# Performance work log

Hardware: AMD Instinct MI355X
Metric: run time of the kernel (lower is better)

The kernel has to match this reference:

```python
import jax, jax.numpy as jnp
import numpy as np

IN_FEATURES = 2048
HIDDEN_DIM = 1024
ENC_DIM = 1024
DEC_DIM = IN_FEATURES - ENC_DIM
MASK_VAL = -50000.0


def setup_inputs() -> dict:
    key = jax.random.key(0)
    k1, k2, k3, k4, k5 = jax.random.split(key, 5)
    B, S = 32, 2048
    encoder_outputs = jax.random.normal(k1, (B, S, ENC_DIM), dtype=jnp.float32)
    decoder_state = jax.random.normal(k2, (B, DEC_DIM), dtype=jnp.float32)
    # lengths in [1, S]
    sequence_length = jax.random.randint(k3, (B,), 1, S + 1).astype(jnp.int64)
    # fc_w: Linear(in_features, hidden_dim, bias=False) -> weight [hidden, in_feat]
    W = jax.random.normal(k4, (HIDDEN_DIM, IN_FEATURES), dtype=jnp.float32) / np.sqrt(IN_FEATURES)
    # fc_v: Linear(hidden_dim, 1, bias=False) -> weight [1, hidden]; store as [hidden]
    v = jax.random.normal(k5, (HIDDEN_DIM,), dtype=jnp.float32) / np.sqrt(HIDDEN_DIM)
    return {"encoder_outputs": encoder_outputs, "sequence_length": sequence_length,
            "decoder_state": decoder_state, "W": W, "v": v}


def reference(encoder_outputs, sequence_length, decoder_state, W, v):
    # score = v^T tanh(W [h; s]) == v^T tanh(W_enc h + W_dec s)  (avoids concat)
    W_enc = W[:, :ENC_DIM]      # [H, De]
    W_dec = W[:, ENC_DIM:]      # [H, Dd]
    # [B, S, H] + [B, 1, H]
    hidden = jnp.tanh(jnp.einsum('bse,he->bsh', encoder_outputs, W_enc)
                      + jnp.einsum('bd,hd->bh', decoder_state, W_dec)[:, None, :])
    logits = jnp.einsum('bsh,h->bs', hidden, v)                      # [B, S]
    S = logits.shape[1]
    mask = jnp.arange(S)[None, :] < sequence_length[:, None]          # [B, S]
    masked_logits = jnp.where(mask, logits, jnp.float32(MASK_VAL))
    attn_weight = jax.nn.softmax(masked_logits, axis=1)               # [B, S]
    out = jnp.einsum('bs,bse->be', attn_weight, encoder_outputs)      # [B, De]
    return (out, attn_weight)
```

## Files before the change

### kernel.cpp

```cpp
#include <hip/hip_runtime.h>
#include <hip/hip_bf16.h>

#define B 32
#define S 2048
#define E 1024
#define H 1024
#define MASK_VAL -50000.0f

typedef __attribute__((ext_vector_type(8))) short bf16x8_t;
typedef __attribute__((ext_vector_type(4))) float f32x4_t;

__device__ __forceinline__ float fast_tanh(float x) {
    float a = fabsf(x);
    float e = __expf(-2.0f * a);
    float t = (1.0f - e) * __builtin_amdgcn_rcpf(1.0f + e);
    return copysignf(t, x);
}

__device__ __forceinline__ float b2f(short s) {
    return __uint_as_float(((unsigned)(unsigned short)s) << 16);
}

__device__ __forceinline__ bf16x8_t cvt8(const float4 f0, const float4 f1) {
    union { bf16x8_t s8; __hip_bfloat162 h[4]; } u;
    u.h[0] = __float22bfloat162_rn(make_float2(f0.x, f0.y));
    u.h[1] = __float22bfloat162_rn(make_float2(f0.z, f0.w));
    u.h[2] = __float22bfloat162_rn(make_float2(f1.x, f1.y));
    u.h[3] = __float22bfloat162_rn(make_float2(f1.z, f1.w));
    return u.s8;
}

__device__ __forceinline__ void gload16(const void* g, void* l) {
    __builtin_amdgcn_global_load_lds(
        (const __attribute__((address_space(1))) void*)g,
        (__attribute__((address_space(3))) void*)l, 16, 0, 0);
}

__global__ __launch_bounds__(256) void kfused0(
    const float* __restrict__ W, const float* __restrict__ dec,
    const float* __restrict__ enc, const int* __restrict__ seq,
    __hip_bfloat16* __restrict__ Wb, float* __restrict__ dec_proj,
    __hip_bfloat16* __restrict__ encb)
{
    int blk = blockIdx.x, tid = threadIdx.x;
    if (blk < 1024) {
        int idx = (blk * 256 + tid) * 4;
        int h = idx >> 10, e = idx & 1023;
        float4 f = *(const float4*)(W + (size_t)h * 2048 + e);
        __hip_bfloat162 p0 = __float22bfloat162_rn(make_float2(f.x, f.y));
        __hip_bfloat162 p1 = __float22bfloat162_rn(make_float2(f.z, f.w));
        *reinterpret_cast<__hip_bfloat162*>(Wb + idx)     = p0;
        *reinterpret_cast<__hip_bfloat162*>(Wb + idx + 2) = p1;
    } else if (blk < 2048) {
        int h = blk - 1024;
        __shared__ float4 wlds[256];
        wlds[tid] = *(const float4*)(W + (size_t)h * 2048 + 1024 + tid * 4);
        __syncthreads();
        int b = tid >> 3, chunk = tid & 7;
        const float4* dd = (const float4*)(dec + b * 1024 + chunk * 128);
        float acc = 0.f;
        #pragma unroll
        for (int i = 0; i < 32; ++i) {
            float4 w4 = wlds[chunk * 32 + i];
            float4 d4 = dd[i];
            acc += w4.x * d4.x + w4.y * d4.y + w4.z * d4.z + w4.w * d4.w;
        }
        acc += __shfl_xor(acc, 1);
        acc += __shfl_xor(acc, 2);
        acc += __shfl_xor(acc, 4);
        if (chunk == 0) dec_proj[b * H + h] = acc;
    } else {
        int g = blk - 2048;
        int c = g & 15, b = g >> 4;
        if (c * 128 >= seq[b]) return;
        size_t base = ((size_t)b * S + c * 128) << 10;
        const float* src = enc + base;
        __hip_bfloat16* dst = encb + base;
        #pragma unroll 4
        for (int it = 0; it < 64; ++it) {
            int idx = it * 2048 + tid * 8;
            float4 f0 = *(const float4*)(src + idx);
            float4 f1 = *(const float4*)(src + idx + 4);
            *(bf16x8_t*)(dst + idx) = cvt8(f0, f1);
        }
    }
}

template<int MODE>
__global__ __launch_bounds__(512, 2) void k2_mfma(
    const float* __restrict__ enc, const __hip_bfloat16* __restrict__ encb,
    const __hip_bfloat16* __restrict__ Wb, const float* __restrict__ v,
    const float* __restrict__ dec_proj, const int* __restrict__ seq,
    float* __restrict__ part)
{
    const int bid  = blockIdx.x;
    const int pair = (bid >> 6) * 8 + (bid & 7);
    const int ht   = (bid >> 3) & 7;
    const int b    = pair >> 4;
    const int s0   = (pair & 15) * 128;
    if (s0 >= seq[b]) return;
    const int h0 = ht * 128;

    const int tid  = threadIdx.x;
    const int wave = tid >> 6;
    const int lane = tid & 63;
    const int wr = wave >> 2, wc = wave & 3;
    const int cr = lane & 15, cg = lane >> 4;

    __shared__ __hip_bfloat16 Al[2][128 * 64];
    __shared__ __hip_bfloat16 Bl[2][128 * 64];

    const int colb  = (tid & 7) * 16;
    const int rbase = tid >> 3;

    f32x4_t acc[4][2];
    #pragma unroll
    for (int m = 0; m < 4; ++m)
        #pragma unroll
        for (int n = 0; n < 2; ++n)
            acc[m][n] = (f32x4_t){0.f, 0.f, 0.f, 0.f};

    auto stage = [&](int buf, int kt) {
        #pragma unroll
        for (int i = 0; i < 2; ++i) {
            const int row   = i * 64 + rbase;
            const int scolb = colb ^ ((row & 7) << 4);
            const __hip_bfloat16* bg =
                Wb + (((size_t)(h0 + row)) << 10) + kt * 64 + (scolb >> 1);
            gload16(bg, (char*)&Bl[buf][0] + (i * 512 + tid) * 16);
            if (MODE == 0) {
                const __hip_bfloat16* ag =
                    encb + (((size_t)b * S + s0 + row) << 10) + kt * 64 + (scolb >> 1);
                gload16(ag, (char*)&Al[buf][0] + (i * 512 + tid) * 16);
            } else {
                const float* af =
                    enc + (((size_t)b * S + s0 + row) << 10) + kt * 64 + (tid & 7) * 8;
                bf16x8_t v8 = cvt8(*(const float4*)af, *(const float4*)(af + 4));
                *(bf16x8_t*)((char*)&Al[buf][0] + row * 128 + scolb) = v8;
            }
        }
    };

    stage(0, 0);
    __syncthreads();
    int cur = 0;
    for (int kt = 0; kt < 16; ++kt) {
        if (kt < 15) stage(cur ^ 1, kt + 1);
        bf16x8_t afr[2][4], bfr[2][2];
        #pragma unroll
        for (int ks = 0; ks < 2; ++ks) {
            #pragma unroll
            for (int m = 0; m < 4; ++m) {
                const int arow  = wr * 64 + m * 16 + cr;
                const int acolb = (ks * 64 + cg * 16) ^ ((arow & 7) << 4);
                afr[ks][m] = *(const bf16x8_t*)((const char*)&Al[cur][0] + arow * 128 + acolb);
            }
            #pragma unroll
            for (int n = 0; n < 2; ++n) {
                const int brow  = wc * 32 + n * 16 + cr;
                const int bcolb = (ks * 64 + cg * 16) ^ ((brow & 7) << 4);
                bfr[ks][n] = *(const bf16x8_t*)((const char*)&Bl[cur][0] + brow * 128 + bcolb);
            }
        }
        #pragma unroll
        for (int ks = 0; ks < 2; ++ks)
            #pragma unroll
            for (int m = 0; m < 4; ++m)
                #pragma unroll
                for (int n = 0; n < 2; ++n)
                    acc[m][n] = __builtin_amdgcn_mfma_f32_16x16x32_bf16(
                        afr[ks][m], bfr[ks][n], acc[m][n], 0, 0, 0);
        __syncthreads();
        cur ^= 1;
    }

    float vv[2], dp[2];
    #pragma unroll
    for (int n = 0; n < 2; ++n) {
        int h = h0 + wc * 32 + n * 16 + cr;
        vv[n] = v[h];
        dp[n] = dec_proj[b * H + h];
    }
    #pragma unroll
    for (int m = 0; m < 4; ++m) {
        #pragma unroll
        for (int j = 0; j < 4; ++j) {
            float t = 0.f;
            #pragma unroll
            for (int n = 0; n < 2; ++n)
                t += vv[n] * fast_tanh(acc[m][n][j] + dp[n]);
            t += __shfl_xor(t, 1);
            t += __shfl_xor(t, 2);
            t += __shfl_xor(t, 4);
            t += __shfl_xor(t, 8);
            if (cr == 0) {
                int srow = s0 + wr * 64 + m * 16 + cg * 4 + j;
                part[(size_t)(b * S + srow) * 32 + ht * 4 + wc] = t;
            }
        }
    }
}

__global__ __launch_bounds__(256) void k3_softmax(
    const float* __restrict__ part, const int* __restrict__ seq,
    float* __restrict__ attn)
{
    int b = blockIdx.x, tid = threadIdx.x;
    int len = seq[b];
    float vals[8];
    float mx = -3.4e38f;
    #pragma unroll
    for (int i = 0; i < 8; ++i) {
        int s = i * 256 + tid;
        float x = MASK_VAL;
        if (s < len) {
            const f32x4_t* p = (const f32x4_t*)&part[(size_t)(b * S + s) * 32];
            float acc = 0.f;
            #pragma unroll
            for (int q = 0; q < 8; ++q) {
                f32x4_t a = p[q];
                acc += (a[0] + a[1]) + (a[2] + a[3]);
            }
            x = acc;
        }
        vals[i] = x;
        mx = fmaxf(mx, x);
    }
    #pragma unroll
    for (int off = 1; off < 64; off <<= 1) mx = fmaxf(mx, __shfl_xor(mx, off));
    __shared__ float red[8];
    int wave = tid >> 6, lane = tid & 63;
    if (lane == 0) red[wave] = mx;
    __syncthreads();
    mx = fmaxf(fmaxf(red[0], red[1]), fmaxf(red[2], red[3]));
    float e[8];
    float sum = 0.f;
    #pragma unroll
    for (int i = 0; i < 8; ++i) { e[i] = __expf(vals[i] - mx); sum += e[i]; }
    #pragma unroll
    for (int off = 1; off < 64; off <<= 1) sum += __shfl_xor(sum, off);
    if (lane == 0) red[4 + wave] = sum;
    __syncthreads();
    sum = red[4] + red[5] + red[6] + red[7];
    float inv = 1.0f / sum;
    #pragma unroll
    for (int i = 0; i < 8; ++i) attn[b * S + i * 256 + tid] = e[i] * inv;
}

template<int AMODE>
__global__ __launch_bounds__(256) void k4_partial(
    const float* __restrict__ enc, const __hip_bfloat16* __restrict__ encb,
    const float* __restrict__ attn, const int* __restrict__ seq,
    float* __restrict__ opart)
{
    int c = blockIdx.x, b = blockIdx.y, tid = threadIdx.x;
    int base_s = c * 128;
    int len = seq[b];
    if (AMODE == 0) {
        int e0 = (tid & 127) * 8;
        int so = tid >> 7;
        float av[8];
        #pragma unroll
        for (int j = 0; j < 8; ++j) av[j] = 0.f;
        if (base_s < len) {
            int s_end = min(128, len - base_s);
            for (int s = so; s < s_end; s += 2) {
                float w = attn[b * S + base_s + s];
                bf16x8_t u = *(const bf16x8_t*)(encb +
                    (((size_t)b * S + base_s + s) << 10) + e0);
                #pragma unroll
                for (int j = 0; j < 8; ++j) av[j] += w * b2f(u[j]);
            }
        }
        float* dst = opart + (((size_t)(b * 16 + c) * 2 + so) << 10) + e0;
        *(float4*)dst       = make_float4(av[0], av[1], av[2], av[3]);
        *(float4*)(dst + 4) = make_float4(av[4], av[5], av[6], av[7]);
    } else {
        float4 acc = make_float4(0.f, 0.f, 0.f, 0.f);
        if (base_s < len) {
            int s_end = min(128, len - base_s);
            const float* ep = enc + (((size_t)b * S + base_s) << 10) + tid * 4;
            const float* ap = attn + b * S + base_s;
            for (int s = 0; s < s_end; ++s) {
                float w = ap[s];
                float4 ev = *(const float4*)ep;
                ep += E;
                acc.x += w * ev.x; acc.y += w * ev.y;
                acc.z += w * ev.z; acc.w += w * ev.w;
            }
        }
        float* dst = opart + (((size_t)(b * 16 + c) * 2) << 10) + tid * 4;
        *(float4*)dst = acc;
        float* dst2 = opart + (((size_t)(b * 16 + c) * 2 + 1) << 10) + tid * 4;
        *(float4*)dst2 = make_float4(0.f, 0.f, 0.f, 0.f);
    }
}

__global__ __launch_bounds__(256) void k5_reduce(
    const float* __restrict__ opart, float* __restrict__ out)
{
    int gid = blockIdx.x * 256 + threadIdx.x;
    int b = gid >> 10, e = gid & 1023;
    float s = 0.f;
    #pragma unroll
    for (int c = 0; c < 32; ++c) s += opart[((size_t)(b * 32 + c) << 10) + e];
    out[gid] = s;
}

extern "C" void kernel_launch(void* const* d_in, const int* in_sizes, int n_in,
                              void* d_out, int out_size, void* d_ws, size_t ws_size,
                              hipStream_t stream)
{
    const float* enc = (const float*)d_in[0];
    const int*   seq = (const int*)d_in[1];
    const float* dec = (const float*)d_in[2];
    const float* W   = (const float*)d_in[3];
    const float* v   = (const float*)d_in[4];

    float* out  = (float*)d_out;
    float* attn = out + B * E;

    float* dec_proj = (float*)d_ws;
    float* part     = dec_proj + B * H;
    float* opart    = part + (size_t)B * S * 32;
    __hip_bfloat16* Wb = (__hip_bfloat16*)(opart + (size_t)B * 32 * 1024);
    __hip_bfloat16* encb = Wb + (size_t)H * E;

    const size_t need = (size_t)(B * H + B * S * 32 + B * 32 * 1024) * 4
                      + (size_t)H * E * 2 + (size_t)B * S * E * 2;
    const bool use_encb = ws_size >= need;

    if (use_encb) {
        hipLaunchKernelGGL(kfused0, dim3(2560), dim3(256), 0, stream,
                           W, dec, enc, seq, Wb, dec_proj, encb);
        hipLaunchKernelGGL(k2_mfma<0>, dim3(4096), dim3(512), 0, stream,
                           enc, encb, Wb, v, dec_proj, seq, part);
    } else {
        hipLaunchKernelGGL(kfused0, dim3(2048), dim3(256), 0, stream,
                           W, dec, enc, seq, Wb, dec_proj, encb);
        hipLaunchKernelGGL(k2_mfma<2>, dim3(4096), dim3(512), 0, stream,
                           enc, encb, Wb, v, dec_proj, seq, part);
    }
    hipLaunchKernelGGL(k3_softmax, dim3(B), dim3(256), 0, stream,
                       part, seq, attn);
    if (use_encb) {
        hipLaunchKernelGGL(k4_partial<0>, dim3(16, B), dim3(256), 0, stream,
                           enc, encb, attn, seq, opart);
    } else {
        hipLaunchKernelGGL(k4_partial<1>, dim3(16, B), dim3(256), 0, stream,
                           enc, encb, attn, seq, opart);
    }
    hipLaunchKernelGGL(k5_reduce, dim3(B * E / 256), dim3(256), 0, stream,
                       opart, out);
}
```

Baseline: 217.0 us.

## Double MFMA kernel block size to 1024 threads with 16-wide per-wave tiles

The score GEMM kernel now runs 16 waves per block instead of 8, each wave computing a 64x16 output tile instead of 64x32. Each thread stages one 16-byte chunk per operand per k-step instead of two, and the partial-logit buffer widens from 32 to 64 columns per row, with softmax summing 16 vec4 chunks. The aim is more waves in flight to hide load latency. In exchange, each wave reloads the A fragments for half as much MFMA work, and the partials buffer doubles.

```diff
diff --git a/kernel.cpp b/kernel.cpp
--- a/kernel.cpp
+++ b/kernel.cpp
@@ -87,7 +87,7 @@
 }
 
 template<int MODE>
-__global__ __launch_bounds__(512, 2) void k2_mfma(
+__global__ __launch_bounds__(1024, 8) void k2_mfma(
     const float* __restrict__ enc, const __hip_bfloat16* __restrict__ encb,
     const __hip_bfloat16* __restrict__ Wb, const float* __restrict__ v,
     const float* __restrict__ dec_proj, const int* __restrict__ seq,
@@ -104,98 +104,77 @@
     const int tid  = threadIdx.x;
     const int wave = tid >> 6;
     const int lane = tid & 63;
-    const int wr = wave >> 2, wc = wave & 3;
+    const int wr = wave >> 3, wc = wave & 7;
     const int cr = lane & 15, cg = lane >> 4;
 
     __shared__ __hip_bfloat16 Al[2][128 * 64];
     __shared__ __hip_bfloat16 Bl[2][128 * 64];
 
-    const int colb  = (tid & 7) * 16;
-    const int rbase = tid >> 3;
-
-    f32x4_t acc[4][2];
+    const int srow_  = tid >> 3;
+    const int scolb_ = ((tid & 7) * 16) ^ ((srow_ & 7) << 4);
+
+    f32x4_t acc[4];
     #pragma unroll
     for (int m = 0; m < 4; ++m)
-        #pragma unroll
-        for (int n = 0; n < 2; ++n)
-            acc[m][n] = (f32x4_t){0.f, 0.f, 0.f, 0.f};
+        acc[m] = (f32x4_t){0.f, 0.f, 0.f, 0.f};
 
     auto stage = [&](int buf, int kt) {
-        #pragma unroll
-        for (int i = 0; i < 2; ++i) {
-            const int row   = i * 64 + rbase;
-            const int scolb = colb ^ ((row & 7) << 4);
-            const __hip_bfloat16* bg =
-                Wb + (((size_t)(h0 + row)) << 10) + kt * 64 + (scolb >> 1);
-            gload16(bg, (char*)&Bl[buf][0] + (i * 512 + tid) * 16);
-            if (MODE == 0) {
-                const __hip_bfloat16* ag =
-                    encb + (((size_t)b * S + s0 + row) << 10) + kt * 64 + (scolb >> 1);
-                gload16(ag, (char*)&Al[buf][0] + (i * 512 + tid) * 16);
-            } else {
-                const float* af =
-                    enc + (((size_t)b * S + s0 + row) << 10) + kt * 64 + (tid & 7) * 8;
-                bf16x8_t v8 = cvt8(*(const float4*)af, *(const float4*)(af + 4));
-                *(bf16x8_t*)((char*)&Al[buf][0] + row * 128 + scolb) = v8;
-            }
+        const __hip_bfloat16* bg =
+            Wb + (((size_t)(h0 + srow_)) << 10) + kt * 64 + (scolb_ >> 1);
+        gload16(bg, (char*)&Bl[buf][0] + tid * 16);
+        if (MODE == 0) {
+            const __hip_bfloat16* ag =
+                encb + (((size_t)b * S + s0 + srow_) << 10) + kt * 64 + (scolb_ >> 1);
+            gload16(ag, (char*)&Al[buf][0] + tid * 16);
+        } else {
+            const float* af =
+                enc + (((size_t)b * S + s0 + srow_) << 10) + kt * 64 + (tid & 7) * 8;
+            bf16x8_t v8 = cvt8(*(const float4*)af, *(const float4*)(af + 4));
+            *(bf16x8_t*)((char*)&Al[buf][0] + srow_ * 128 + scolb_) = v8;
         }
     };
 
     stage(0, 0);
     __syncthreads();
     int cur = 0;
+    const int brow  = wc * 16 + cr;
     for (int kt = 0; kt < 16; ++kt) {
         if (kt < 15) stage(cur ^ 1, kt + 1);
-        bf16x8_t afr[2][4], bfr[2][2];
         #pragma unroll
         for (int ks = 0; ks < 2; ++ks) {
+            bf16x8_t afr[4], bfr;
             #pragma unroll
             for (int m = 0; m < 4; ++m) {
                 const int arow  = wr * 64 + m * 16 + cr;
                 const int acolb = (ks * 64 + cg * 16) ^ ((arow & 7) << 4);
-                afr[ks][m] = *(const bf16x8_t*)((const char*)&Al[cur][0] + arow * 128 + acolb);
-            }
-            #pragma unroll
-            for (int n = 0; n < 2; ++n) {
-                const int brow  = wc * 32 + n * 16 + cr;
-                const int bcolb = (ks * 64 + cg * 16) ^ ((brow & 7) << 4);
-                bfr[ks][n] = *(const bf16x8_t*)((const char*)&Bl[cur][0] + brow * 128 + bcolb);
-            }
-        }
-        #pragma unroll
-        for (int ks = 0; ks < 2; ++ks)
+                afr[m] = *(const bf16x8_t*)((const char*)&Al[cur][0] + arow * 128 + acolb);
+            }
+            const int bcolb = (ks * 64 + cg * 16) ^ ((brow & 7) << 4);
+            bfr = *(const bf16x8_t*)((const char*)&Bl[cur][0] + brow * 128 + bcolb);
             #pragma unroll
             for (int m = 0; m < 4; ++m)
-                #pragma unroll
-                for (int n = 0; n < 2; ++n)
-                    acc[m][n] = __builtin_amdgcn_mfma_f32_16x16x32_bf16(
-                        afr[ks][m], bfr[ks][n], acc[m][n], 0, 0, 0);
+                acc[m] = __builtin_amdgcn_mfma_f32_16x16x32_bf16(
+                    afr[m], bfr, acc[m], 0, 0, 0);
+        }
         __syncthreads();
         cur ^= 1;
     }
 
-    float vv[2], dp[2];
-    #pragma unroll
-    for (int n = 0; n < 2; ++n) {
-        int h = h0 + wc * 32 + n * 16 + cr;
-        vv[n] = v[h];
-        dp[n] = dec_proj[b * H + h];
-    }
+    const int h = h0 + wc * 16 + cr;
+    const float vv = v[h];
+    const float dp = dec_proj[b * H + h];
     #pragma unroll
     for (int m = 0; m < 4; ++m) {
         #pragma unroll
         for (int j = 0; j < 4; ++j) {
-            float t = 0.f;
-            #pragma unroll
-            for (int n = 0; n < 2; ++n)
-                t += vv[n] * fast_tanh(acc[m][n][j] + dp[n]);
+            float t = vv * fast_tanh(acc[m][j] + dp);
             t += __shfl_xor(t, 1);
             t += __shfl_xor(t, 2);
             t += __shfl_xor(t, 4);
             t += __shfl_xor(t, 8);
             if (cr == 0) {
                 int srow = s0 + wr * 64 + m * 16 + cg * 4 + j;
-                part[(size_t)(b * S + srow) * 32 + ht * 4 + wc] = t;
+                part[(size_t)(b * S + srow) * 64 + ht * 8 + wc] = t;
             }
         }
     }
@@ -214,10 +193,10 @@
         int s = i * 256 + tid;
         float x = MASK_VAL;
         if (s < len) {
-            const f32x4_t* p = (const f32x4_t*)&part[(size_t)(b * S + s) * 32];
+            const f32x4_t* p = (const f32x4_t*)&part[(size_t)(b * S + s) * 64];
             float acc = 0.f;
             #pragma unroll
-            for (int q = 0; q < 8; ++q) {
+            for (int q = 0; q < 16; ++q) {
                 f32x4_t a = p[q];
                 acc += (a[0] + a[1]) + (a[2] + a[3]);
             }
@@ -322,23 +301,23 @@
 
     float* dec_proj = (float*)d_ws;
     float* part     = dec_proj + B * H;
-    float* opart    = part + (size_t)B * S * 32;
+    float* opart    = part + (size_t)B * S * 64;
     __hip_bfloat16* Wb = (__hip_bfloat16*)(opart + (size_t)B * 32 * 1024);
     __hip_bfloat16* encb = Wb + (size_t)H * E;
 
-    const size_t need = (size_t)(B * H + B * S * 32 + B * 32 * 1024) * 4
+    const size_t need = (size_t)(B * H + (size_t)B * S * 64 + B * 32 * 1024) * 4
                       + (size_t)H * E * 2 + (size_t)B * S * E * 2;
     const bool use_encb = ws_size >= need;
 
     if (use_encb) {
         hipLaunchKernelGGL(kfused0, dim3(2560), dim3(256), 0, stream,
                            W, dec, enc, seq, Wb, dec_proj, encb);
-        hipLaunchKernelGGL(k2_mfma<0>, dim3(4096), dim3(512), 0, stream,
+        hipLaunchKernelGGL(k2_mfma<0>, dim3(4096), dim3(1024), 0, stream,
                            enc, encb, Wb, v, dec_proj, seq, part);
     } else {
         hipLaunchKernelGGL(kfused0, dim3(2048), dim3(256), 0, stream,
                            W, dec, enc, seq, Wb, dec_proj, encb);
-        hipLaunchKernelGGL(k2_mfma<2>, dim3(4096), dim3(512), 0, stream,
+        hipLaunchKernelGGL(k2_mfma<2>, dim3(4096), dim3(1024), 0, stream,
                            enc, encb, Wb, v, dec_proj, seq, part);
     }
     hipLaunchKernelGGL(k3_softmax, dim3(B), dim3(256), 0, stream,
```

New measurement: 248.5 us. 1.15x slower.
